# Kernel optimization log

Measured on AMD Instinct MI355X. Metric: run time of the kernel, lower is better.

Reference implementation:

```python
import jax, jax.numpy as jnp
import numpy as np

B, S, HID = 1, 2048, 4096
NH, NKV, HD = 32, 8, 128
GROUPS = NH // NKV
ROPE_THETA = 10000.0


def rotate_half(x):
    x1, x2 = jnp.split(x, 2, axis=-1)
    return jnp.concatenate([-x2, x1], axis=-1)


def rope_cos_sin(position_ids, head_dim, dtype):
    # inv_freq: [hd/2]; position_ids: [B, S]
    inv_freq = 1.0 / (ROPE_THETA ** (jnp.arange(0, head_dim, 2, dtype=jnp.float32) / head_dim))
    freqs = position_ids.astype(jnp.float32)[..., None] * inv_freq  # [B, S, hd/2]
    emb = jnp.concatenate([freqs, freqs], axis=-1)                  # [B, S, hd]
    return jnp.cos(emb).astype(dtype), jnp.sin(emb).astype(dtype)


def apply_rope(x, cos, sin):
    # x: [B, H, S, hd]; cos/sin: [B, S, hd] -> broadcast over heads
    return x * cos[:, None] + rotate_half(x) * sin[:, None]


def setup_inputs() -> dict:
    key = jax.random.key(0)
    ks = jax.random.split(key, 5)
    scale = 0.02
    return {
        "hidden_states": jax.random.normal(ks[0], (B, S, HID), dtype=jnp.float32),
        "wq": jax.random.normal(ks[1], (HID, NH * HD), dtype=jnp.float32) * scale,
        "wk": jax.random.normal(ks[2], (HID, NKV * HD), dtype=jnp.float32) * scale,
        "wv": jax.random.normal(ks[3], (HID, NKV * HD), dtype=jnp.float32) * scale,
        "wo": jax.random.normal(ks[4], (NH * HD, HID), dtype=jnp.float32) * scale,
        "position_ids": jnp.arange(S, dtype=jnp.int32)[None, :],
    }


def reference(hidden_states, wq, wk, wv, wo, position_ids):
    bsz, q_len, _ = hidden_states.shape
    # projections (nn.Linear, bias=False)
    q = (hidden_states @ wq).reshape(bsz, q_len, NH, HD).transpose(0, 2, 1, 3)   # [B,NH,S,hd]
    k = (hidden_states @ wk).reshape(bsz, q_len, NKV, HD).transpose(0, 2, 1, 3)  # [B,NKV,S,hd]
    v = (hidden_states @ wv).reshape(bsz, q_len, NKV, HD).transpose(0, 2, 1, 3)
    # RoPE applied to Q and K at global positions (prefill: no past cache)
    cos, sin = rope_cos_sin(position_ids, HD, q.dtype)
    q = apply_rope(q, cos, sin)
    k = apply_rope(k, cos, sin)
    # GQA: expand KV heads to query heads
    k_full = jnp.repeat(k, GROUPS, axis=1)  # [B,NH,S,hd]
    v_full = jnp.repeat(v, GROUPS, axis=1)
    # prefill flash attention == causal SDPA
    logits = jnp.einsum('bhqd,bhkd->bhqk', q, k_full) / jnp.sqrt(jnp.asarray(HD, q.dtype))
    causal = jnp.tril(jnp.ones((q_len, q_len), dtype=bool))
    neg = jnp.asarray(jnp.finfo(q.dtype).min, q.dtype)
    logits = jnp.where(causal[None, None], logits, neg)
    probs = jax.nn.softmax(logits, axis=-1)                     # [B,NH,S,S]
    attn = jnp.einsum('bhqk,bhkd->bhqd', probs, v_full)          # [B,NH,S,hd]
    attn_output = attn.transpose(0, 2, 1, 3).reshape(bsz, q_len, NH * HD) @ wo
    # chunked prefill eviction scores: causal attention probs accumulated over
    # all queries, aggregated per KV head group -> [B, NKV, kv_len]
    accumulated_scores = probs.sum(axis=2).reshape(bsz, NKV, GROUPS, q_len).sum(axis=2)
    return attn_output, accumulated_scores
```

## Files before the change

kernel.cpp:

```cpp
#include <hip/hip_runtime.h>
#include <hip/hip_bf16.h>
#include <cstdint>
#include <cstddef>

#define S_LEN 2048
#define HID_DIM 4096
#define NH 32
#define NKV 8
#define HD 128
#define LOG2E 1.4426950408889634f
#define SCALE 0.08838834764831845f

typedef __attribute__((ext_vector_type(8))) short bf16x8;
typedef __attribute__((ext_vector_type(4))) float f32x4;
typedef __attribute__((ext_vector_type(4))) short short4v;
typedef __attribute__((ext_vector_type(4))) unsigned u32x4;

__device__ __forceinline__ short f2bf(float f) {
  union { float f; unsigned u; } v; v.f = f;
  return (short)((v.u + 0x7fffu + ((v.u >> 16) & 1u)) >> 16);
}
__device__ __forceinline__ float bf2f(short s) {
  union { unsigned u; float f; } v; v.u = ((unsigned)(unsigned short)s) << 16;
  return v.f;
}
__device__ __forceinline__ unsigned cvt_pk_bf16(float lo, float hi) {
  unsigned r;
  asm("v_cvt_pk_bf16_f32 %0, %1, %2" : "=v"(r) : "v"(lo), "v"(hi));
  return r;
}
__device__ __forceinline__ void gld_lds16(const void* g, void* l) {
  __builtin_amdgcn_global_load_lds((const __attribute__((address_space(1))) unsigned*)g,
                                   (__attribute__((address_space(3))) unsigned*)l, 16, 0, 0);
}

#define WAITVM4() asm volatile("s_waitcnt vmcnt(4)" ::: "memory")
#define WAITVM2() asm volatile("s_waitcnt vmcnt(2)" ::: "memory")
#define WAITVM0() asm volatile("s_waitcnt vmcnt(0)" ::: "memory")

__global__ void cvt_kernel(const float* __restrict__ in, short* __restrict__ out, int n) {
  int i = (blockIdx.x * 256 + threadIdx.x) * 4;
  if (i < n) {
    float4 f = *(const float4*)(in + i);
    short4v o = { f2bf(f.x), f2bf(f.y), f2bf(f.z), f2bf(f.w) };
    *(short4v*)(out + i) = o;
  }
}

__global__ void tconv_kernel(const float* __restrict__ in, short* __restrict__ out, int R, int C) {
  __shared__ float tile[32][33];
  int tr = blockIdx.y * 32, tc = blockIdx.x * 32;
  int tx = threadIdx.x & 31, ty = threadIdx.x >> 5;
#pragma unroll
  for (int i = 0; i < 32; i += 8)
    tile[ty + i][tx] = in[(size_t)(tr + ty + i) * C + tc + tx];
  __syncthreads();
#pragma unroll
  for (int i = 0; i < 32; i += 8)
    out[(size_t)(tc + ty + i) * R + tr + tx] = f2bf(tile[tx][ty + i]);
}

template<int MODE>
__global__ __launch_bounds__(256, 2) void gemm_bt_kernel(
    const short* __restrict__ A, const short* __restrict__ Bt,
    void* __restrict__ Cout, int M, int N, int K, int nbx)
{
  __shared__ short As[128 * 32];
  __shared__ short Bs[128 * 32];
  const int tid = threadIdx.x;
  const int lane = tid & 63;
  const int w = tid >> 6;
  const int wm = w >> 1, wn = w & 1;
  const int q8 = gridDim.x >> 3;
  const int lin = (blockIdx.x & 7) * q8 + (blockIdx.x >> 3);
  const int by = lin / nbx, bx = lin - by * nbx;
  const int m0 = by * 128, n0 = bx * 128;

  f32x4 acc[4][4];
#pragma unroll
  for (int i = 0; i < 4; i++)
#pragma unroll
    for (int j = 0; j < 4; j++) acc[i][j] = (f32x4){0.f, 0.f, 0.f, 0.f};

  for (int k0 = 0; k0 < K; k0 += 32) {
    __syncthreads();
#pragma unroll
    for (int rep = 0; rep < 2; rep++) {
      int c = rep * 256 + w * 64 + lane;
      int row = c >> 2, slot = c & 3;
      int gs = slot ^ (row & 3);
      gld_lds16(A + (size_t)(m0 + row) * K + k0 + gs * 8, As + c * 8);
      gld_lds16(Bt + (size_t)(n0 + row) * K + k0 + gs * 8, Bs + c * 8);
    }
    __syncthreads();
    bf16x8 af[4], bf[4];
#pragma unroll
    for (int ms = 0; ms < 4; ms++) {
      int row = wm * 64 + ms * 16 + (lane & 15);
      af[ms] = *(const bf16x8*)(As + row * 32 + (((lane >> 4) ^ (row & 3)) << 3));
    }
#pragma unroll
    for (int ns = 0; ns < 4; ns++) {
      int row = wn * 64 + ns * 16 + (lane & 15);
      bf[ns] = *(const bf16x8*)(Bs + row * 32 + (((lane >> 4) ^ (row & 3)) << 3));
    }
#pragma unroll
    for (int ms = 0; ms < 4; ms++)
#pragma unroll
      for (int ns = 0; ns < 4; ns++)
        acc[ms][ns] = __builtin_amdgcn_mfma_f32_16x16x32_bf16(af[ms], bf[ns], acc[ms][ns], 0, 0, 0);
  }

#pragma unroll
  for (int ms = 0; ms < 4; ms++) {
    int mb = m0 + wm * 64 + ms * 16 + ((lane >> 4) << 2);
#pragma unroll
    for (int ns = 0; ns < 4; ns++) {
      int n = n0 + wn * 64 + ns * 16 + (lane & 15);
      if (MODE == 3) {
        short* o = (short*)Cout;
        if (n < NH * HD) {
          int head = n >> 7, d = n & 127;
#pragma unroll
          for (int r = 0; r < 4; r++)
            o[((size_t)head * M + (mb + r)) * HD + d] = f2bf(acc[ms][ns][r]);
        } else if (n < (NH + NKV) * HD) {
          int head = (n - NH * HD) >> 7, d = n & 127;
          short* ok = o + (size_t)NH * S_LEN * HD;
#pragma unroll
          for (int r = 0; r < 4; r++)
            ok[((size_t)head * M + (mb + r)) * HD + d] = f2bf(acc[ms][ns][r]);
        } else {
          int head = (n - (NH + NKV) * HD) >> 7, d = n & 127;
          short* ov = o + (size_t)(NH + NKV) * S_LEN * HD;
          short4v pk;
#pragma unroll
          for (int r = 0; r < 4; r++) pk[r] = f2bf(acc[ms][ns][r]);
          *(short4v*)(ov + ((size_t)head * HD + d) * M + mb) = pk;
        }
      } else {
        float* o = (float*)Cout;
#pragma unroll
        for (int r = 0; r < 4; r++)
          o[(size_t)(mb + r) * N + n] = acc[ms][ns][r];
      }
    }
  }
}

__global__ void rope_kernel(short* __restrict__ q, short* __restrict__ k,
                            const int* __restrict__ pos_ids) {
  const int s = blockIdx.x;
  const int hh = blockIdx.y * 4 + threadIdx.y;
  const int d = threadIdx.x;
  const float pos = (float)pos_ids[s];
  const float inv = __expf(-(float)d * 0.14391157f);
  float sn, c;
  __sincosf(pos * inv, &sn, &c);
  short* base = (hh < NH) ? (q + ((size_t)hh * S_LEN + s) * HD)
                          : (k + ((size_t)(hh - NH) * S_LEN + s) * HD);
  float x1 = bf2f(base[d]), x2 = bf2f(base[d + 64]);
  base[d] = f2bf(x1 * c - x2 * sn);
  base[d + 64] = f2bf(x2 * c + x1 * sn);
}

__global__ __launch_bounds__(512, 2) void attn_kernel(
    const short* __restrict__ Qr, const short* __restrict__ Kr, const short* __restrict__ Vt,
    short* __restrict__ attn_out, float* __restrict__ scores)
{
  __shared__ short Ks[2][64 * 128];
  __shared__ short Vs[2][128 * 64];
  __shared__ float cs[2048];

  const int tid = threadIdx.x;
  const int lane = tid & 63;
  const int w = tid >> 6;
  const int hi = lane >> 4;
  const int ql = lane & 15;
  const int lin = (blockIdx.x & 7) * 32 + (blockIdx.x >> 3);
  const int h = lin >> 3;
  const int pr = lin & 7;
  const int kvh = h >> 2;
  const float CS = SCALE * LOG2E;

  const short* KrB = Kr + (size_t)kvh * S_LEN * HD;
  const short* VtB = Vt + (size_t)kvh * HD * S_LEN;

  for (int i = tid; i < 2048; i += 512) cs[i] = 0.f;

  auto stageKV = [&](int bb, int t) {
    const int kb2 = t * 64;
#pragma unroll
    for (int rep = 0; rep < 2; rep++) {
      int c = rep * 512 + tid;
      int x = c >> 4, slot = c & 15;
      int key = (x & 32) | ((x & 16) >> 2) | ((x & 12) << 1) | (x & 3);
      int gs = slot ^ (x & 7);
      gld_lds16(KrB + (size_t)(kb2 + key) * HD + gs * 8, &Ks[bb][c * 8]);
    }
#pragma unroll
    for (int rep = 0; rep < 2; rep++) {
      int c = rep * 512 + tid;
      int d = c >> 3, slot = c & 7;
      int gs = slot ^ (d & 7);
      gld_lds16(VtB + (size_t)d * S_LEN + kb2 + gs * 8, &Vs[bb][c * 8]);
    }
  };
  auto stageK = [&](int bb, int t) {
    const int kb2 = t * 64;
#pragma unroll
    for (int rep = 0; rep < 2; rep++) {
      int c = rep * 512 + tid;
      int x = c >> 4, slot = c & 15;
      int key = (x & 32) | ((x & 16) >> 2) | ((x & 12) << 1) | (x & 3);
      int gs = slot ^ (x & 7);
      gld_lds16(KrB + (size_t)(kb2 + key) * HD + gs * 8, &Ks[bb][c * 8]);
    }
  };

  int maxnt = 0;

  for (int sidx = 0; sidx < 2; sidx++) {
    const int qt = sidx ? (15 - pr) : pr;
    const int nt = 2 * qt + 2;
    if (nt > maxnt) maxnt = nt;
    const int qbase = qt * 128 + w * 16;
    const int qglob = qbase + ql;
    const int qmax = qbase + 15;

    bf16x8 qf[4];
    {
      const short* qrow = Qr + ((size_t)h * S_LEN + qglob) * HD + hi * 8;
#pragma unroll
      for (int kc = 0; kc < 4; kc++) qf[kc] = *(const bf16x8*)(qrow + kc * 32);
    }

    f32x4 oacc[8];
#pragma unroll
    for (int i = 0; i < 8; i++) oacc[i] = (f32x4){0.f, 0.f, 0.f, 0.f};
    float lsum = 0.f;

    stageKV(0, 0);
    for (int t = 0; t < nt; t++) {
      const int b = t & 1;
      const int kb = t * 64;
      if (t + 1 < nt) { stageKV(b ^ 1, t + 1); WAITVM4(); }
      else            { WAITVM0(); }
      __builtin_amdgcn_s_barrier();

      if (kb <= qmax) {
        f32x4 sf[4];
#pragma unroll
        for (int g = 0; g < 4; g++) sf[g] = (f32x4){0.f, 0.f, 0.f, 0.f};
        __builtin_amdgcn_s_setprio(1);
#pragma unroll
        for (int g = 0; g < 4; g++)
#pragma unroll
          for (int kc = 0; kc < 4; kc++) {
            int row = g * 16 + ql;
            bf16x8 kf = *(const bf16x8*)(&Ks[b][row * 128 + (((kc * 4 + hi) ^ (ql & 7)) << 3)]);
            sf[g] = __builtin_amdgcn_mfma_f32_16x16x32_bf16(kf, qf[kc], sf[g], 0, 0, 0);
          }
        __builtin_amdgcn_s_setprio(0);

        float p[4][4];
#pragma unroll
        for (int g = 0; g < 4; g++)
#pragma unroll
          for (int r = 0; r < 4; r++) p[g][r] = exp2f(sf[g][r] * CS);
        if (kb + 63 > qbase) {
#pragma unroll
          for (int g = 0; g < 4; g++)
#pragma unroll
            for (int r = 0; r < 4; r++) {
              int key = kb + ((g >> 1) << 5) + ((g & 1) << 2) + (hi << 3) + r;
              if (key > qglob) p[g][r] = 0.f;
            }
        }
#pragma unroll
        for (int g = 0; g < 4; g++)
#pragma unroll
          for (int r = 0; r < 4; r++) lsum += p[g][r];

        bf16x8 pa[2];
#pragma unroll
        for (int kh = 0; kh < 2; kh++) {
          u32x4 pw;
          pw[0] = cvt_pk_bf16(p[2 * kh][0], p[2 * kh][1]);
          pw[1] = cvt_pk_bf16(p[2 * kh][2], p[2 * kh][3]);
          pw[2] = cvt_pk_bf16(p[2 * kh + 1][0], p[2 * kh + 1][1]);
          pw[3] = cvt_pk_bf16(p[2 * kh + 1][2], p[2 * kh + 1][3]);
          pa[kh] = __builtin_bit_cast(bf16x8, pw);
        }

        __builtin_amdgcn_s_setprio(1);
#pragma unroll
        for (int ds = 0; ds < 8; ds++) {
          int d = ds * 16 + ql;
#pragma unroll
          for (int kh = 0; kh < 2; kh++) {
            bf16x8 vf = *(const bf16x8*)(&Vs[b][d * 64 + (((kh * 4 + hi) ^ (d & 7)) << 3)]);
            oacc[ds] = __builtin_amdgcn_mfma_f32_16x16x32_bf16(pa[kh], vf, oacc[ds], 0, 0, 0);
          }
        }
        __builtin_amdgcn_s_setprio(0);
      }
      __builtin_amdgcn_s_barrier();
    }

    lsum += __shfl_xor(lsum, 16);
    lsum += __shfl_xor(lsum, 32);
    float rl[4];
#pragma unroll
    for (int r = 0; r < 4; r++) rl[r] = 1.f / __shfl(lsum, hi * 4 + r);

#pragma unroll
    for (int ds = 0; ds < 8; ds++)
#pragma unroll
      for (int r = 0; r < 4; r++) {
        int qq = qbase + hi * 4 + r;
        int d = ds * 16 + ql;
        attn_out[(size_t)qq * HID_DIM + h * HD + d] = f2bf(oacc[ds][r] * rl[r]);
      }

    stageK(0, 0);
    for (int t = 0; t < nt; t++) {
      const int b = t & 1;
      const int kb = t * 64;
      if (t + 1 < nt) { stageK(b ^ 1, t + 1); WAITVM2(); }
      else            { WAITVM0(); }
      __builtin_amdgcn_s_barrier();

      if (kb <= qmax) {
        f32x4 sg[4];
#pragma unroll
        for (int c = 0; c < 4; c++) sg[c] = (f32x4){0.f, 0.f, 0.f, 0.f};
        __builtin_amdgcn_s_setprio(1);
#pragma unroll
        for (int c = 0; c < 4; c++)
#pragma unroll
          for (int kc = 0; kc < 4; kc++) {
            int row = c * 16 + ql;
            bf16x8 kf = *(const bf16x8*)(&Ks[b][row * 128 + (((kc * 4 + hi) ^ (ql & 7)) << 3)]);
            sg[c] = __builtin_amdgcn_mfma_f32_16x16x32_bf16(qf[kc], kf, sg[c], 0, 0, 0);
          }
        __builtin_amdgcn_s_setprio(0);

        const bool diag = (kb + 63 > qbase);
#pragma unroll
        for (int c = 0; c < 4; c++) {
          int key = kb + ((c >> 1) << 5) + ((c & 1) << 2) + ((ql >> 2) << 3) + (ql & 3);
          float sum = 0.f;
          if (diag) {
#pragma unroll
            for (int r = 0; r < 4; r++) {
              float pv = exp2f(sg[c][r] * CS) * rl[r];
              if (key > qbase + hi * 4 + r) pv = 0.f;
              sum += pv;
            }
          } else {
#pragma unroll
            for (int r = 0; r < 4; r++) sum += exp2f(sg[c][r] * CS) * rl[r];
          }
          sum += __shfl_xor(sum, 16);
          sum += __shfl_xor(sum, 32);
          if (lane < 16) atomicAdd(&cs[key], sum);
        }
      }
      __builtin_amdgcn_s_barrier();
    }
  }

  __builtin_amdgcn_s_barrier();
  const int nk = maxnt * 64;
  for (int i = tid; i < nk; i += 512)
    atomicAdd(scores + (size_t)kvh * S_LEN + i, cs[i]);
}

extern "C" void kernel_launch(void* const* d_in, const int* in_sizes, int n_in,
                              void* d_out, int out_size, void* d_ws, size_t ws_size,
                              hipStream_t stream) {
  const float* hs = (const float*)d_in[0];
  const float* wq = (const float*)d_in[1];
  const float* wk = (const float*)d_in[2];
  const float* wv = (const float*)d_in[3];
  const float* wo = (const float*)d_in[4];
  const int* pos = (const int*)d_in[5];
  float* out = (float*)d_out;

  char* ws = (char*)d_ws;
  const size_t off_hs   = 0;
  const size_t off_wqT  = off_hs   + (size_t)S_LEN * HID_DIM * 2;
  const size_t off_wkT  = off_wqT  + (size_t)HID_DIM * HID_DIM * 2;
  const size_t off_wvT  = off_wkT  + (size_t)1024 * HID_DIM * 2;
  const size_t off_woT  = off_wvT  + (size_t)1024 * HID_DIM * 2;
  const size_t off_Qr   = off_woT  + (size_t)HID_DIM * HID_DIM * 2;
  const size_t off_Kr   = off_Qr   + (size_t)NH * S_LEN * HD * 2;
  const size_t off_Vt   = off_Kr   + (size_t)NKV * S_LEN * HD * 2;
  const size_t off_attn = off_Vt   + (size_t)NKV * HD * S_LEN * 2;

  short* hsb  = (short*)(ws + off_hs);
  short* wqT  = (short*)(ws + off_wqT);
  short* wkT  = (short*)(ws + off_wkT);
  short* wvT  = (short*)(ws + off_wvT);
  short* woT  = (short*)(ws + off_woT);
  short* Qr   = (short*)(ws + off_Qr);
  short* Kr   = (short*)(ws + off_Kr);
  short* Vt   = (short*)(ws + off_Vt);
  short* attb = (short*)(ws + off_attn);

  cvt_kernel<<<dim3((S_LEN * HID_DIM) / 1024), 256, 0, stream>>>(hs, hsb, S_LEN * HID_DIM);
  tconv_kernel<<<dim3(128, 128), 256, 0, stream>>>(wq, wqT, HID_DIM, HID_DIM);
  tconv_kernel<<<dim3(32, 128), 256, 0, stream>>>(wk, wkT, HID_DIM, 1024);
  tconv_kernel<<<dim3(32, 128), 256, 0, stream>>>(wv, wvT, HID_DIM, 1024);
  tconv_kernel<<<dim3(128, 128), 256, 0, stream>>>(wo, woT, HID_DIM, HID_DIM);

  gemm_bt_kernel<3><<<768, 256, 0, stream>>>(hsb, wqT, Qr, S_LEN, 6144, HID_DIM, 48);

  rope_kernel<<<dim3(S_LEN, 10), dim3(64, 4), 0, stream>>>(Qr, Kr, pos);

  hipMemsetAsync(out + (size_t)S_LEN * HID_DIM, 0, (size_t)NKV * S_LEN * sizeof(float), stream);
  attn_kernel<<<256, 512, 0, stream>>>(Qr, Kr, Vt, attb, out + (size_t)S_LEN * HID_DIM);

  gemm_bt_kernel<2><<<512, 256, 0, stream>>>(attb, woT, out, S_LEN, HID_DIM, HID_DIM, 32);
}
```

Measured before the change: 398.7 us.

## Double-buffer GEMM LDS tiles and remap blocks to XCD-local 2D chunks

The projection GEMM kernel now uses two LDS buffers, issuing the global-to-LDS loads for the next K tile before computing on the current one, with vmcnt waits and raw barriers in place of two __syncthreads per iteration. Block-to-tile mapping is changed so each of the 8 XCDs owns a contiguous rectangle of output tiles (rchunk x cchunk), aiming for better L2 reuse of A and B rows. Launch bounds rise to 4 blocks per CU. Doubling LDS and raising the occupancy target may push register pressure or cause spills, and the WAITVM counts must match the number of outstanding loads for correctness.

```diff
diff --git a/kernel.cpp b/kernel.cpp
--- a/kernel.cpp
+++ b/kernel.cpp
@@ -61,54 +61,65 @@
 }
 
 template<int MODE>
-__global__ __launch_bounds__(256, 2) void gemm_bt_kernel(
+__global__ __launch_bounds__(256, 4) void gemm_bt_kernel(
     const short* __restrict__ A, const short* __restrict__ Bt,
-    void* __restrict__ Cout, int M, int N, int K, int nbx)
+    void* __restrict__ Cout, int M, int N, int K, int rchunk, int cchunk)
 {
-  __shared__ short As[128 * 32];
-  __shared__ short Bs[128 * 32];
+  __shared__ short As[2][128 * 32];
+  __shared__ short Bs[2][128 * 32];
   const int tid = threadIdx.x;
   const int lane = tid & 63;
   const int w = tid >> 6;
   const int wm = w >> 1, wn = w & 1;
-  const int q8 = gridDim.x >> 3;
-  const int lin = (blockIdx.x & 7) * q8 + (blockIdx.x >> 3);
-  const int by = lin / nbx, bx = lin - by * nbx;
+  const int xcd = blockIdx.x & 7;
+  const int local = blockIdx.x >> 3;
+  const int by = (xcd >> 2) * rchunk + (local % rchunk);
+  const int bx = (xcd & 3) * cchunk + (local / rchunk);
   const int m0 = by * 128, n0 = bx * 128;
 
-  f32x4 acc[4][4];
-#pragma unroll
-  for (int i = 0; i < 4; i++)
-#pragma unroll
-    for (int j = 0; j < 4; j++) acc[i][j] = (f32x4){0.f, 0.f, 0.f, 0.f};
-
-  for (int k0 = 0; k0 < K; k0 += 32) {
-    __syncthreads();
+  auto stage = [&](int bb, int k0) {
 #pragma unroll
     for (int rep = 0; rep < 2; rep++) {
-      int c = rep * 256 + w * 64 + lane;
+      int c = rep * 256 + tid;
       int row = c >> 2, slot = c & 3;
       int gs = slot ^ (row & 3);
-      gld_lds16(A + (size_t)(m0 + row) * K + k0 + gs * 8, As + c * 8);
-      gld_lds16(Bt + (size_t)(n0 + row) * K + k0 + gs * 8, Bs + c * 8);
-    }
-    __syncthreads();
+      gld_lds16(A + (size_t)(m0 + row) * K + k0 + gs * 8, &As[bb][c * 8]);
+      gld_lds16(Bt + (size_t)(n0 + row) * K + k0 + gs * 8, &Bs[bb][c * 8]);
+    }
+  };
+
+  f32x4 acc[4][4];
+#pragma unroll
+  for (int i = 0; i < 4; i++)
+#pragma unroll
+    for (int j = 0; j < 4; j++) acc[i][j] = (f32x4){0.f, 0.f, 0.f, 0.f};
+
+  const int NT = K >> 5;
+  stage(0, 0);
+  for (int kt = 0; kt < NT; kt++) {
+    const int b = kt & 1;
+    if (kt + 1 < NT) { stage(b ^ 1, (kt + 1) << 5); WAITVM4(); }
+    else             { WAITVM0(); }
+    __builtin_amdgcn_s_barrier();
+
     bf16x8 af[4], bf[4];
 #pragma unroll
     for (int ms = 0; ms < 4; ms++) {
       int row = wm * 64 + ms * 16 + (lane & 15);
-      af[ms] = *(const bf16x8*)(As + row * 32 + (((lane >> 4) ^ (row & 3)) << 3));
+      af[ms] = *(const bf16x8*)(&As[b][row * 32 + (((lane >> 4) ^ (row & 3)) << 3)]);
     }
 #pragma unroll
     for (int ns = 0; ns < 4; ns++) {
       int row = wn * 64 + ns * 16 + (lane & 15);
-      bf[ns] = *(const bf16x8*)(Bs + row * 32 + (((lane >> 4) ^ (row & 3)) << 3));
+      bf[ns] = *(const bf16x8*)(&Bs[b][row * 32 + (((lane >> 4) ^ (row & 3)) << 3)]);
     }
 #pragma unroll
     for (int ms = 0; ms < 4; ms++)
 #pragma unroll
       for (int ns = 0; ns < 4; ns++)
         acc[ms][ns] = __builtin_amdgcn_mfma_f32_16x16x32_bf16(af[ms], bf[ns], acc[ms][ns], 0, 0, 0);
+
+    __builtin_amdgcn_s_barrier();
   }
 
 #pragma unroll
@@ -415,12 +426,12 @@
   tconv_kernel<<<dim3(32, 128), 256, 0, stream>>>(wv, wvT, HID_DIM, 1024);
   tconv_kernel<<<dim3(128, 128), 256, 0, stream>>>(wo, woT, HID_DIM, HID_DIM);
 
-  gemm_bt_kernel<3><<<768, 256, 0, stream>>>(hsb, wqT, Qr, S_LEN, 6144, HID_DIM, 48);
+  gemm_bt_kernel<3><<<768, 256, 0, stream>>>(hsb, wqT, Qr, S_LEN, 6144, HID_DIM, 8, 12);
 
   rope_kernel<<<dim3(S_LEN, 10), dim3(64, 4), 0, stream>>>(Qr, Kr, pos);
 
   hipMemsetAsync(out + (size_t)S_LEN * HID_DIM, 0, (size_t)NKV * S_LEN * sizeof(float), stream);
   attn_kernel<<<256, 512, 0, stream>>>(Qr, Kr, Vt, attb, out + (size_t)S_LEN * HID_DIM);
 
-  gemm_bt_kernel<2><<<512, 256, 0, stream>>>(attb, woT, out, S_LEN, HID_DIM, HID_DIM, 32);
-}
+  gemm_bt_kernel<2><<<512, 256, 0, stream>>>(attb, woT, out, S_LEN, HID_DIM, HID_DIM, 8, 8);
+}
```

Result: faster. 386.7 us (-3.0%).
